# Optimization experiments

Hardware: AMD Instinct MI355X
Metric: run time of the kernel (lower is better)

The kernel has to match this reference:

```python
import jax, jax.numpy as jnp
import numpy as np

N = 100000
E = 1600000
DIN, DH, DOUT = 128, 128, 64


def setup_inputs() -> dict:
    key = jax.random.key(0)
    ks = jax.random.split(key, 9)
    x = jax.random.normal(ks[0], (N, DIN), dtype=jnp.float32)
    src = jax.random.randint(ks[1], (E,), 0, N, dtype=jnp.int32)
    dst = jax.random.randint(ks[2], (E,), 0, N, dtype=jnp.int32)
    edge_index = jnp.stack([src, dst])  # [2, E]

    def glorot(k, fi, fo):
        return jax.random.normal(k, (fi, fo), jnp.float32) * (1.0 / np.sqrt(fi))

    return {
        "x": x,
        "edge_index": edge_index,
        "W1": glorot(ks[3], DIN, DH), "b1": jnp.zeros((DH,), jnp.float32),
        "W2": glorot(ks[4], DH, DH),  "b2": jnp.zeros((DH,), jnp.float32),
        "W3": glorot(ks[5], DH, DOUT), "b3": jnp.zeros((DOUT,), jnp.float32),
    }


def _norm_and_edges(edge_index):
    # GCNConv: add self-loops, symmetric normalization D^{-1/2} (A+I) D^{-1/2}
    loop = jnp.arange(N, dtype=edge_index.dtype)
    src = jnp.concatenate([edge_index[0], loop])  # [E+N]
    dst = jnp.concatenate([edge_index[1], loop])
    deg = jax.ops.segment_sum(jnp.ones_like(dst, jnp.float32), dst, num_segments=N)
    dinv = jnp.where(deg > 0, jax.lax.rsqrt(jnp.maximum(deg, 1.0)), 0.0)
    norm = dinv[src] * dinv[dst]  # [E+N]
    return src, dst, norm


def _gcn_conv(x, W, b, src, dst, norm):
    h = x @ W                                   # [N, dout]
    msg = h[src] * norm[:, None]                # gather + scale over edges
    agg = jax.ops.segment_sum(msg, dst, num_segments=N)
    return agg + b


def reference(x, edge_index, W1, b1, W2, b2, W3, b3):
    src, dst, norm = _norm_and_edges(edge_index)
    out = []
    h = jax.nn.relu(_gcn_conv(x, W1, b1, src, dst, norm))
    out.append(h)
    h = jax.nn.relu(_gcn_conv(h, W2, b2, src, dst, norm))
    out.append(h)
    y = _gcn_conv(h, W3, b3, src, dst, norm)
    return (y, *out)
```

## Files before the change

kernel.cpp:

```cpp
#include <hip/hip_runtime.h>
#include <math.h>


typedef __attribute__((ext_vector_type(8))) short bfrag8;
typedef __attribute__((ext_vector_type(4))) float ffrag4;

__device__ __forceinline__ unsigned short f2bf(float f) {
  unsigned u = __float_as_uint(f);
  return (unsigned short)((u + 0x7FFFu + ((u >> 16) & 1u)) >> 16);
}
__device__ __forceinline__ float bfLo(unsigned v) { return __uint_as_float(v << 16); }
__device__ __forceinline__ float bfHi(unsigned v) { return __uint_as_float(v & 0xFFFF0000u); }


__global__ __launch_bounds__(256) void k_zero(int* __restrict__ cnt,
                                              int* __restrict__ fillPos, int n) {
  int i = blockIdx.x * blockDim.x + threadIdx.x;
  if (i < n) { cnt[i] = 0; fillPos[i] = 0; }
}

__global__ __launch_bounds__(256) void k_deg(const int* __restrict__ dst,
                                             int* __restrict__ cnt, int E) {
  int i = blockIdx.x * blockDim.x + threadIdx.x;
  int stride = gridDim.x * blockDim.x;
  for (; i < E; i += stride) atomicAdd(&cnt[dst[i]], 1);
}

__global__ __launch_bounds__(256) void k_dinv(const int* __restrict__ cnt,
                                              float* __restrict__ dinv, int n) {
  int i = blockIdx.x * blockDim.x + threadIdx.x;
  if (i < n) dinv[i] = rsqrtf(1.0f + (float)cnt[i]);
}

__global__ __launch_bounds__(256) void k_scan1(const int* __restrict__ cnt,
                                               int* __restrict__ exc,
                                               int* __restrict__ bsum, int n) {
  __shared__ int lds[256];
  int t = threadIdx.x;
  int base = blockIdx.x * 1024 + t * 4;
  int v0 = (base + 0 < n) ? cnt[base + 0] : 0;
  int v1 = (base + 1 < n) ? cnt[base + 1] : 0;
  int v2 = (base + 2 < n) ? cnt[base + 2] : 0;
  int v3 = (base + 3 < n) ? cnt[base + 3] : 0;
  int sum = v0 + v1 + v2 + v3;
  lds[t] = sum;
  __syncthreads();
  for (int off = 1; off < 256; off <<= 1) {
    int val = lds[t];
    if (t >= off) val += lds[t - off];
    __syncthreads();
    lds[t] = val;
    __syncthreads();
  }
  int ex = lds[t] - sum;
  if (base + 0 < n) exc[base + 0] = ex;
  ex += v0;
  if (base + 1 < n) exc[base + 1] = ex;
  ex += v1;
  if (base + 2 < n) exc[base + 2] = ex;
  ex += v2;
  if (base + 3 < n) exc[base + 3] = ex;
  if (t == 255) bsum[blockIdx.x] = lds[255];
}

__global__ __launch_bounds__(128) void k_scan2(int* __restrict__ bsum, int nb) {
  __shared__ int lds[128];
  int t = threadIdx.x;
  int v = (t < nb) ? bsum[t] : 0;
  lds[t] = v;
  __syncthreads();
  for (int off = 1; off < 128; off <<= 1) {
    int val = lds[t];
    if (t >= off) val += lds[t - off];
    __syncthreads();
    lds[t] = val;
    __syncthreads();
  }
  if (t < nb) bsum[t] = lds[t] - v;
}

__global__ __launch_bounds__(256) void k_scan3(int* __restrict__ exc,
                                               const int* __restrict__ bsum, int n) {
  int i = blockIdx.x * blockDim.x + threadIdx.x;
  if (i < n) exc[i] += bsum[i >> 10];
}

__global__ __launch_bounds__(256) void k_fill8(const int* __restrict__ src,
                                               const int* __restrict__ dst,
                                               const int* __restrict__ rowStart,
                                               int* __restrict__ fillPos,
                                               int* __restrict__ eSrc,
                                               int E, int rsize) {
  const int range = blockIdx.x & 7;
  const int sub = blockIdx.x >> 3;
  const int nSub = gridDim.x >> 3;
  const int lo = range * rsize, hi = lo + rsize;
  int i = sub * blockDim.x + threadIdx.x;
  const int stride = nSub * blockDim.x;
  for (; i < E; i += stride) {
    int d = dst[i];
    if (d >= lo && d < hi) {
      int p = rowStart[d] + atomicAdd(&fillPos[d], 1);
      eSrc[p] = src[i];
    }
  }
}


__global__ __launch_bounds__(256) void k_scale(const float* __restrict__ h,
                                               const float* __restrict__ dinv,
                                               uint4* __restrict__ s4, int nQuads) {
  int i = blockIdx.x * blockDim.x + threadIdx.x;
  int stride = gridDim.x * blockDim.x;
  for (; i < nQuads; i += stride) {
    int row = i >> 4;
    int q = i & 15;
    float dv = dinv[row];
    const float4* hp = (const float4*)&h[(size_t)row * 128 + 8 * q];
    float4 a = hp[0], b = hp[1];
    uint4 o;
    o.x = (unsigned)f2bf(dv * a.x) | ((unsigned)f2bf(dv * a.y) << 16);
    o.y = (unsigned)f2bf(dv * a.z) | ((unsigned)f2bf(dv * a.w) << 16);
    o.z = (unsigned)f2bf(dv * b.x) | ((unsigned)f2bf(dv * b.y) << 16);
    o.w = (unsigned)f2bf(dv * b.z) | ((unsigned)f2bf(dv * b.w) << 16);
    s4[i] = o;
  }
}

__global__ __launch_bounds__(256, 8) void k_agg(const unsigned* __restrict__ sU,
                                                const float* __restrict__ dinv,
                                                const int* __restrict__ eSrc,
                                                const int* __restrict__ rowStart,
                                                const int* __restrict__ cnt,
                                                unsigned* __restrict__ tB, int n) {
  const int wid = threadIdx.x >> 6, lane = threadIdx.x & 63;
  const int half = lane >> 5, sl = lane & 31;
  for (int node = blockIdx.x * 4 + wid; node < n; node += gridDim.x * 4) {
    const int st = rowStart[node], c = cnt[node];
    const int* es = eSrc + st;
    const float dv = dinv[node];
    uint2 vs = *(const uint2*)&sU[(size_t)node * 64 + 2 * sl];
    float a0, a1, a2, a3;
    if (half == 0) {
      a0 = bfLo(vs.x); a1 = bfHi(vs.x); a2 = bfLo(vs.y); a3 = bfHi(vs.y);
    } else {
      a0 = a1 = a2 = a3 = 0.f;
    }
    const int cl = c < 64 ? c : 64;
    int myIdx = (lane < cl) ? es[lane] : 0;
    int j = 0;
    for (; j + 8 <= cl; j += 8) {
      int iA0 = __shfl(myIdx, j + 0), iB0 = __shfl(myIdx, j + 1);
      int iA1 = __shfl(myIdx, j + 2), iB1 = __shfl(myIdx, j + 3);
      int iA2 = __shfl(myIdx, j + 4), iB2 = __shfl(myIdx, j + 5);
      int iA3 = __shfl(myIdx, j + 6), iB3 = __shfl(myIdx, j + 7);
      int x0 = half ? iB0 : iA0;
      int x1 = half ? iB1 : iA1;
      int x2 = half ? iB2 : iA2;
      int x3 = half ? iB3 : iA3;
      uint2 v0 = *(const uint2*)&sU[(size_t)x0 * 64 + 2 * sl];
      uint2 v1 = *(const uint2*)&sU[(size_t)x1 * 64 + 2 * sl];
      uint2 v2 = *(const uint2*)&sU[(size_t)x2 * 64 + 2 * sl];
      uint2 v3 = *(const uint2*)&sU[(size_t)x3 * 64 + 2 * sl];
      a0 += bfLo(v0.x); a1 += bfHi(v0.x); a2 += bfLo(v0.y); a3 += bfHi(v0.y);
      a0 += bfLo(v1.x); a1 += bfHi(v1.x); a2 += bfLo(v1.y); a3 += bfHi(v1.y);
      a0 += bfLo(v2.x); a1 += bfHi(v2.x); a2 += bfLo(v2.y); a3 += bfHi(v2.y);
      a0 += bfLo(v3.x); a1 += bfHi(v3.x); a2 += bfLo(v3.y); a3 += bfHi(v3.y);
    }
    for (; j < c; j += 2) {
      int iA = (j < cl) ? __shfl(myIdx, j) : es[j];
      int hasB = (j + 1 < c);
      int iB = hasB ? ((j + 1 < cl) ? __shfl(myIdx, j + 1) : es[j + 1]) : iA;
      int x = half ? iB : iA;
      uint2 v = *(const uint2*)&sU[(size_t)x * 64 + 2 * sl];
      if (half && !hasB) { v.x = 0u; v.y = 0u; }
      a0 += bfLo(v.x); a1 += bfHi(v.x); a2 += bfLo(v.y); a3 += bfHi(v.y);
    }
    a0 += __shfl_xor(a0, 32);
    a1 += __shfl_xor(a1, 32);
    a2 += __shfl_xor(a2, 32);
    a3 += __shfl_xor(a3, 32);
    if (half == 0) {
      uint2 o;
      o.x = (unsigned)f2bf(dv * a0) | ((unsigned)f2bf(dv * a1) << 16);
      o.y = (unsigned)f2bf(dv * a2) | ((unsigned)f2bf(dv * a3) << 16);
      *(uint2*)&tB[(size_t)node * 64 + 2 * sl] = o;
    }
  }
}

template <int NFO, bool RELU, bool WRITE_S>
__global__ __launch_bounds__(256) void k_gemmM(const unsigned* __restrict__ tB,
                                               const float* __restrict__ W,
                                               const float* __restrict__ bias,
                                               const float* __restrict__ dinv,
                                               float* __restrict__ out,
                                               unsigned* __restrict__ sNext, int n) {
  __shared__ unsigned short Wt[NFO * 128];
  for (int t = threadIdx.x; t < 128 * NFO; t += 256) {
    int k = t / NFO, c = t % NFO;
    int hs = (k >> 2) ^ (c & 7);
    Wt[c * 128 + hs * 4 + (k & 3)] = f2bf(W[t]);
  }
  __syncthreads();
  const int wid = threadIdx.x >> 6, lane = threadIdx.x & 63;
  const int r16 = lane & 15;
  const int q4 = lane >> 4;
  const int NT = NFO / 16;
  for (int node0 = (blockIdx.x * 4 + wid) * 16; node0 < n;
       node0 += gridDim.x * 4 * 16) {
    if (node0 + 16 <= n) {
      const unsigned* trow = tB + (size_t)(node0 + r16) * 64;
      union { uint2 u2[2]; bfrag8 v; } Af[4];
      #pragma unroll
      for (int kc = 0; kc < 4; kc++) {
        Af[kc].u2[0] = *(const uint2*)&trow[kc * 16 + 2 * q4];
        Af[kc].u2[1] = *(const uint2*)&trow[kc * 16 + 8 + 2 * q4];
      }
      float dvr[4];
      if (WRITE_S) {
        #pragma unroll
        for (int r = 0; r < 4; r++) dvr[r] = dinv[node0 + q4 * 4 + r];
      }
      #pragma unroll
      for (int ct = 0; ct < NT; ct++) {
        const int col = 16 * ct + r16;
        const int cbase = col * 128;
        const int csw = col & 7;
        ffrag4 acc = {0.f, 0.f, 0.f, 0.f};
        #pragma unroll
        for (int kc = 0; kc < 4; kc++) {
          int h0 = kc * 8 + q4;
          union { uint2 u2[2]; bfrag8 v; } Bf;
          Bf.u2[0] = *(const uint2*)&Wt[cbase + ((h0) ^ csw) * 4];
          Bf.u2[1] = *(const uint2*)&Wt[cbase + ((h0 + 4) ^ csw) * 4];
          acc = __builtin_amdgcn_mfma_f32_16x16x32_bf16(Af[kc].v, Bf.v, acc,
                                                        0, 0, 0);
        }
        float bb = bias[col];
        #pragma unroll
        for (int r = 0; r < 4; r++) {
          int node = node0 + q4 * 4 + r;
          float v = acc[r] + bb;
          if (RELU) v = fmaxf(v, 0.f);
          out[(size_t)node * NFO + col] = v;
          if (WRITE_S) {
            float sv = dvr[r] * v;
            float pv = __shfl_xor(sv, 1);
            if ((lane & 1) == 0)
              sNext[(size_t)node * 64 + (col >> 1)] =
                  (unsigned)f2bf(sv) | ((unsigned)f2bf(pv) << 16);
          }
        }
      }
    } else {
      for (int idx = lane; idx < 16 * NFO; idx += 64) {
        int node = node0 + idx / NFO;
        if (node < n) {
          int col = idx % NFO;
          float acc = 0.f;
          for (int k = 0; k < 128; k++) {
            unsigned tw = tB[(size_t)node * 64 + (k >> 1)];
            float tv = (k & 1) ? bfHi(tw) : bfLo(tw);
            int hs = (k >> 2) ^ (col & 7);
            unsigned short wv = Wt[col * 128 + hs * 4 + (k & 3)];
            acc = fmaf(tv, __uint_as_float(((unsigned)wv) << 16), acc);
          }
          float v = acc + bias[col];
          if (RELU) v = fmaxf(v, 0.f);
          out[(size_t)node * NFO + col] = v;
          if (WRITE_S) {
            unsigned short* sh = (unsigned short*)sNext;
            sh[(size_t)node * 128 + col] = f2bf(dinv[node] * v);
          }
        }
      }
    }
  }
}


template <int NFO, bool RELU>
__global__ __launch_bounds__(512) void k_layer_f32(const float* __restrict__ in,
                                                   const float* __restrict__ W,
                                                   const float* __restrict__ bias,
                                                   const float* __restrict__ dinv,
                                                   const int* __restrict__ eSrc,
                                                   const int* __restrict__ rowStart,
                                                   const int* __restrict__ cnt,
                                                   float* __restrict__ out, int n) {
  __shared__ float Wl[128 * NFO];
  for (int t = threadIdx.x; t < 128 * NFO; t += 512) Wl[t] = W[t];
  __syncthreads();
  const int wid = threadIdx.x >> 6, lane = threadIdx.x & 63;
  for (int node = blockIdx.x * 8 + wid; node < n; node += gridDim.x * 8) {
    const int s = rowStart[node], c = cnt[node];
    const int* es = eSrc + s;
    const float dv = dinv[node];
    float2 x2 = *(const float2*)&in[(size_t)node * 128 + 2 * lane];
    float ax = dv * x2.x, ay = dv * x2.y;
    int j = 0;
    for (; j + 4 <= c; j += 4) {
      int s0 = es[j], s1 = es[j + 1], s2 = es[j + 2], s3 = es[j + 3];
      float d0 = dinv[s0], d1 = dinv[s1], d2 = dinv[s2], d3 = dinv[s3];
      float2 v0 = *(const float2*)&in[(size_t)s0 * 128 + 2 * lane];
      float2 v1 = *(const float2*)&in[(size_t)s1 * 128 + 2 * lane];
      float2 v2 = *(const float2*)&in[(size_t)s2 * 128 + 2 * lane];
      float2 v3 = *(const float2*)&in[(size_t)s3 * 128 + 2 * lane];
      ax = fmaf(d0, v0.x, ax); ay = fmaf(d0, v0.y, ay);
      ax = fmaf(d1, v1.x, ax); ay = fmaf(d1, v1.y, ay);
      ax = fmaf(d2, v2.x, ax); ay = fmaf(d2, v2.y, ay);
      ax = fmaf(d3, v3.x, ax); ay = fmaf(d3, v3.y, ay);
    }
    for (; j < c; j++) {
      int sj = es[j];
      float dj = dinv[sj];
      float2 v = *(const float2*)&in[(size_t)sj * 128 + 2 * lane];
      ax = fmaf(dj, v.x, ax); ay = fmaf(dj, v.y, ay);
    }
    ax *= dv; ay *= dv;
    if constexpr (NFO == 128) {
      float o0 = 0.f, o1 = 0.f;
      #pragma unroll 4
      for (int kk = 0; kk < 64; kk++) {
        float xa = __shfl(ax, kk);
        float xb = __shfl(ay, kk);
        float2 wA = *(const float2*)&Wl[(2 * kk) * 128 + 2 * lane];
        float2 wB = *(const float2*)&Wl[(2 * kk + 1) * 128 + 2 * lane];
        o0 = fmaf(xa, wA.x, o0); o1 = fmaf(xa, wA.y, o1);
        o0 = fmaf(xb, wB.x, o0); o1 = fmaf(xb, wB.y, o1);
      }
      float2 bb = *(const float2*)&bias[2 * lane];
      float r0 = o0 + bb.x, r1 = o1 + bb.y;
      if (RELU) { r0 = fmaxf(r0, 0.f); r1 = fmaxf(r1, 0.f); }
      *(float2*)&out[(size_t)node * 128 + 2 * lane] = make_float2(r0, r1);
    } else {
      float o0 = 0.f;
      #pragma unroll 4
      for (int kk = 0; kk < 64; kk++) {
        float xa = __shfl(ax, kk);
        float xb = __shfl(ay, kk);
        o0 = fmaf(xa, Wl[(2 * kk) * NFO + lane], o0);
        o0 = fmaf(xb, Wl[(2 * kk + 1) * NFO + lane], o0);
      }
      float r0 = o0 + bias[lane];
      if (RELU) r0 = fmaxf(r0, 0.f);
      out[(size_t)node * NFO + lane] = r0;
    }
  }
}


extern "C" void kernel_launch(void* const* d_in, const int* in_sizes, int n_in,
                              void* d_out, int out_size, void* d_ws, size_t ws_size,
                              hipStream_t stream) {
  const float* x  = (const float*)d_in[0];
  const int*   ei = (const int*)d_in[1];
  const float* W1 = (const float*)d_in[2];
  const float* b1 = (const float*)d_in[3];
  const float* W2 = (const float*)d_in[4];
  const float* b2 = (const float*)d_in[5];
  const float* W3 = (const float*)d_in[6];
  const float* b3 = (const float*)d_in[7];

  const int N = in_sizes[0] / 128;
  const int E = in_sizes[1] / 2;
  const int* src = ei;
  const int* dst = ei + E;

  char* ws = (char*)d_ws;
  size_t off = 0;
  auto alloc = [&](size_t bytes) -> void* {
    void* p = ws + off;
    off = (off + bytes + 255) & ~(size_t)255;
    return p;
  };
  int*   cnt      = (int*)alloc((size_t)N * 4);
  int*   fillPos  = (int*)alloc((size_t)N * 4);
  int*   rowStart = (int*)alloc((size_t)N * 4);
  float* dinv     = (float*)alloc((size_t)N * 4);
  int*   bsum     = (int*)alloc(512);
  int*   eSrc     = (int*)alloc((size_t)E * 4);
  unsigned* sU    = (unsigned*)alloc((size_t)N * 64 * 4);
  unsigned* tB    = (unsigned*)alloc((size_t)N * 64 * 4);
  const bool fast = (ws_size >= off);

  float* y    = (float*)d_out;
  float* out1 = y + (size_t)N * 64;
  float* out2 = out1 + (size_t)N * 128;

  k_zero<<<(N + 255) / 256, 256, 0, stream>>>(cnt, fillPos, N);
  k_deg<<<2048, 256, 0, stream>>>(dst, cnt, E);
  k_dinv<<<(N + 255) / 256, 256, 0, stream>>>(cnt, dinv, N);
  int nChunks = (N + 1023) / 1024;
  k_scan1<<<nChunks, 256, 0, stream>>>(cnt, rowStart, bsum, N);
  k_scan2<<<1, 128, 0, stream>>>(bsum, nChunks);
  k_scan3<<<(N + 255) / 256, 256, 0, stream>>>(rowStart, bsum, N);
  const int rsize = (N + 7) / 8;
  k_fill8<<<2048, 256, 0, stream>>>(src, dst, rowStart, fillPos, eSrc, E, rsize);

  if (fast) {
    const int aggBlocks = (N + 3) / 4;
    const int tiles = (N + 15) / 16;
    const int gmBlocks = (tiles + 3) / 4;
    k_scale<<<(N * 16 + 255) / 256, 256, 0, stream>>>(x, dinv, (uint4*)sU, N * 16);
    k_agg<<<aggBlocks, 256, 0, stream>>>(sU, dinv, eSrc, rowStart, cnt, tB, N);
    k_gemmM<128, true, true><<<gmBlocks, 256, 0, stream>>>(tB, W1, b1, dinv, out1, sU, N);
    k_agg<<<aggBlocks, 256, 0, stream>>>(sU, dinv, eSrc, rowStart, cnt, tB, N);
    k_gemmM<128, true, true><<<gmBlocks, 256, 0, stream>>>(tB, W2, b2, dinv, out2, sU, N);
    k_agg<<<aggBlocks, 256, 0, stream>>>(sU, dinv, eSrc, rowStart, cnt, tB, N);
    k_gemmM<64, false, false><<<gmBlocks, 256, 0, stream>>>(tB, W3, b3, dinv, y, nullptr, N);
  } else {
    k_layer_f32<128, true ><<<1024, 512, 0, stream>>>(x,    W1, b1, dinv, eSrc, rowStart, cnt, out1, N);
    k_layer_f32<128, true ><<<1024, 512, 0, stream>>>(out1, W2, b2, dinv, eSrc, rowStart, cnt, out2, N);
    k_layer_f32<64,  false><<<1024, 512, 0, stream>>>(out2, W3, b3, dinv, eSrc, rowStart, cnt, y,    N);
  }
}
```

Before: 439.0 us.

## Pre-bucket edges by destination range and XCD before degree count and CSR fill

```diff
diff --git a/kernel.cpp b/kernel.cpp
--- a/kernel.cpp
+++ b/kernel.cpp
@@ -4,6 +4,8 @@
 
 typedef __attribute__((ext_vector_type(8))) short bfrag8;
 typedef __attribute__((ext_vector_type(4))) float ffrag4;
+
+static constexpr int BCAP = 32768;
 
 __device__ __forceinline__ unsigned short f2bf(float f) {
   unsigned u = __float_as_uint(f);
@@ -19,11 +21,111 @@
   if (i < n) { cnt[i] = 0; fillPos[i] = 0; }
 }
 
-__global__ __launch_bounds__(256) void k_deg(const int* __restrict__ dst,
-                                             int* __restrict__ cnt, int E) {
+__global__ __launch_bounds__(256) void k_zctr(int* __restrict__ c, int m) {
   int i = blockIdx.x * blockDim.x + threadIdx.x;
-  int stride = gridDim.x * blockDim.x;
-  for (; i < E; i += stride) atomicAdd(&cnt[dst[i]], 1);
+  if (i < m) c[i] = 0;
+}
+
+__global__ __launch_bounds__(256) void k_bucket(const int* __restrict__ src,
+                                                const int* __restrict__ dst,
+                                                uint2* __restrict__ buckets,
+                                                uint2* __restrict__ spill,
+                                                int* __restrict__ ctr,
+                                                int E, float invR) {
+  const int xcd = blockIdx.x & 7;
+  const int lane = threadIdx.x & 63;
+  int i = blockIdx.x * blockDim.x + threadIdx.x;
+  int iw = i - lane;
+  const int stride = gridDim.x * blockDim.x;
+  for (; iw < E; iw += stride, i += stride) {
+    bool valid = i < E;
+    int d = 0, s = 0, r = -1;
+    if (valid) {
+      d = dst[i];
+      s = src[i];
+      r = (int)((float)d * invR);
+      r = r > 7 ? 7 : r;
+    }
+    #pragma unroll
+    for (int rr = 0; rr < 8; rr++) {
+      unsigned long long m = __ballot(valid && (r == rr));
+      if (m) {
+        int cnum = __builtin_popcountll(m);
+        int leader = __builtin_ctzll(m);
+        int base = 0;
+        if (lane == leader) base = atomicAdd(&ctr[(rr * 8 + xcd) * 16], cnum);
+        base = __shfl(base, leader);
+        if (valid && r == rr) {
+          int off = __builtin_popcountll(m & ((1ull << lane) - 1ull));
+          int pos = base + off;
+          if (pos < BCAP) {
+            buckets[(size_t)(rr * 8 + xcd) * BCAP + pos] =
+                make_uint2((unsigned)s, (unsigned)d);
+          } else {
+            int sp = atomicAdd(&ctr[64 * 16], 1);
+            spill[sp] = make_uint2((unsigned)s, (unsigned)d);
+          }
+        }
+      }
+    }
+  }
+}
+
+__global__ __launch_bounds__(256) void k_deg8b(const uint2* __restrict__ buckets,
+                                               const uint2* __restrict__ spill,
+                                               const int* __restrict__ ctr,
+                                               int* __restrict__ cnt, float invR) {
+  const int range = blockIdx.x & 7;
+  const int sub = blockIdx.x >> 3;
+  const int nSub = gridDim.x >> 3;
+  const int tid = sub * blockDim.x + threadIdx.x;
+  const int stride = nSub * blockDim.x;
+  #pragma unroll
+  for (int x = 0; x < 8; x++) {
+    int m = ctr[(range * 8 + x) * 16];
+    m = m > BCAP ? BCAP : m;
+    const uint2* b = buckets + (size_t)(range * 8 + x) * BCAP;
+    for (int i = tid; i < m; i += stride) atomicAdd(&cnt[b[i].y], 1);
+  }
+  int sm = ctr[64 * 16];
+  for (int i = tid; i < sm; i += stride) {
+    unsigned d = spill[i].y;
+    int r = (int)((float)d * invR); r = r > 7 ? 7 : r;
+    if (r == range) atomicAdd(&cnt[d], 1);
+  }
+}
+
+__global__ __launch_bounds__(256) void k_fill8b(const uint2* __restrict__ buckets,
+                                                const uint2* __restrict__ spill,
+                                                const int* __restrict__ ctr,
+                                                const int* __restrict__ rowStart,
+                                                int* __restrict__ fillPos,
+                                                int* __restrict__ eSrc, float invR) {
+  const int range = blockIdx.x & 7;
+  const int sub = blockIdx.x >> 3;
+  const int nSub = gridDim.x >> 3;
+  const int tid = sub * blockDim.x + threadIdx.x;
+  const int stride = nSub * blockDim.x;
+  #pragma unroll
+  for (int x = 0; x < 8; x++) {
+    int m = ctr[(range * 8 + x) * 16];
+    m = m > BCAP ? BCAP : m;
+    const uint2* b = buckets + (size_t)(range * 8 + x) * BCAP;
+    for (int i = tid; i < m; i += stride) {
+      uint2 e = b[i];
+      int p = rowStart[e.y] + atomicAdd(&fillPos[e.y], 1);
+      eSrc[p] = (int)e.x;
+    }
+  }
+  int sm = ctr[64 * 16];
+  for (int i = tid; i < sm; i += stride) {
+    uint2 e = spill[i];
+    int r = (int)((float)e.y * invR); r = r > 7 ? 7 : r;
+    if (r == range) {
+      int p = rowStart[e.y] + atomicAdd(&fillPos[e.y], 1);
+      eSrc[p] = (int)e.x;
+    }
+  }
 }
 
 __global__ __launch_bounds__(256) void k_dinv(const int* __restrict__ cnt,
@@ -83,27 +185,6 @@
                                                const int* __restrict__ bsum, int n) {
   int i = blockIdx.x * blockDim.x + threadIdx.x;
   if (i < n) exc[i] += bsum[i >> 10];
-}
-
-__global__ __launch_bounds__(256) void k_fill8(const int* __restrict__ src,
-                                               const int* __restrict__ dst,
-                                               const int* __restrict__ rowStart,
-                                               int* __restrict__ fillPos,
-                                               int* __restrict__ eSrc,
-                                               int E, int rsize) {
-  const int range = blockIdx.x & 7;
-  const int sub = blockIdx.x >> 3;
-  const int nSub = gridDim.x >> 3;
-  const int lo = range * rsize, hi = lo + rsize;
-  int i = sub * blockDim.x + threadIdx.x;
-  const int stride = nSub * blockDim.x;
-  for (; i < E; i += stride) {
-    int d = dst[i];
-    if (d >= lo && d < hi) {
-      int p = rowStart[d] + atomicAdd(&fillPos[d], 1);
-      eSrc[p] = src[i];
-    }
-  }
 }
 
 
@@ -380,26 +461,34 @@
   int*   rowStart = (int*)alloc((size_t)N * 4);
   float* dinv     = (float*)alloc((size_t)N * 4);
   int*   bsum     = (int*)alloc(512);
+  int*   ctr      = (int*)alloc((64 * 16 + 16) * 4);
   int*   eSrc     = (int*)alloc((size_t)E * 4);
   unsigned* sU    = (unsigned*)alloc((size_t)N * 64 * 4);
   unsigned* tB    = (unsigned*)alloc((size_t)N * 64 * 4);
   const bool fast = (ws_size >= off);
 
+  uint2* buckets = (uint2*)tB;
+  uint2* spill   = (uint2*)sU;
+
   float* y    = (float*)d_out;
   float* out1 = y + (size_t)N * 64;
   float* out2 = out1 + (size_t)N * 128;
 
-  k_zero<<<(N + 255) / 256, 256, 0, stream>>>(cnt, fillPos, N);
-  k_deg<<<2048, 256, 0, stream>>>(dst, cnt, E);
-  k_dinv<<<(N + 255) / 256, 256, 0, stream>>>(cnt, dinv, N);
-  int nChunks = (N + 1023) / 1024;
-  k_scan1<<<nChunks, 256, 0, stream>>>(cnt, rowStart, bsum, N);
-  k_scan2<<<1, 128, 0, stream>>>(bsum, nChunks);
-  k_scan3<<<(N + 255) / 256, 256, 0, stream>>>(rowStart, bsum, N);
   const int rsize = (N + 7) / 8;
-  k_fill8<<<2048, 256, 0, stream>>>(src, dst, rowStart, fillPos, eSrc, E, rsize);
+  const float invR = (float)(1.0 / (double)rsize);
 
   if (fast) {
+    k_zero<<<(N + 255) / 256, 256, 0, stream>>>(cnt, fillPos, N);
+    k_zctr<<<5, 256, 0, stream>>>(ctr, 64 * 16 + 16);
+    k_bucket<<<2048, 256, 0, stream>>>(src, dst, buckets, spill, ctr, E, invR);
+    k_deg8b<<<2048, 256, 0, stream>>>(buckets, spill, ctr, cnt, invR);
+    k_dinv<<<(N + 255) / 256, 256, 0, stream>>>(cnt, dinv, N);
+    int nChunks = (N + 1023) / 1024;
+    k_scan1<<<nChunks, 256, 0, stream>>>(cnt, rowStart, bsum, N);
+    k_scan2<<<1, 128, 0, stream>>>(bsum, nChunks);
+    k_scan3<<<(N + 255) / 256, 256, 0, stream>>>(rowStart, bsum, N);
+    k_fill8b<<<2048, 256, 0, stream>>>(buckets, spill, ctr, rowStart, fillPos,
+                                       eSrc, invR);
     const int aggBlocks = (N + 3) / 4;
     const int tiles = (N + 15) / 16;
     const int gmBlocks = (tiles + 3) / 4;
@@ -411,6 +500,17 @@
     k_agg<<<aggBlocks, 256, 0, stream>>>(sU, dinv, eSrc, rowStart, cnt, tB, N);
     k_gemmM<64, false, false><<<gmBlocks, 256, 0, stream>>>(tB, W3, b3, dinv, y, nullptr, N);
   } else {
+    k_zero<<<(N + 255) / 256, 256, 0, stream>>>(cnt, fillPos, N);
+    k_zctr<<<5, 256, 0, stream>>>(ctr, 64 * 16 + 16);
+    k_bucket<<<2048, 256, 0, stream>>>(src, dst, buckets, spill, ctr, E, invR);
+    k_deg8b<<<2048, 256, 0, stream>>>(buckets, spill, ctr, cnt, invR);
+    k_dinv<<<(N + 255) / 256, 256, 0, stream>>>(cnt, dinv, N);
+    int nChunks = (N + 1023) / 1024;
+    k_scan1<<<nChunks, 256, 0, stream>>>(cnt, rowStart, bsum, N);
+    k_scan2<<<1, 128, 0, stream>>>(bsum, nChunks);
+    k_scan3<<<(N + 255) / 256, 256, 0, stream>>>(rowStart, bsum, N);
+    k_fill8b<<<2048, 256, 0, stream>>>(buckets, spill, ctr, rowStart, fillPos,
+                                       eSrc, invR);
     k_layer_f32<128, true ><<<1024, 512, 0, stream>>>(x,    W1, b1, dinv, eSrc, rowStart, cnt, out1, N);
     k_layer_f32<128, true ><<<1024, 512, 0, stream>>>(out1, W2, b2, dinv, eSrc, rowStart, cnt, out2, N);
     k_layer_f32<64,  false><<<1024, 512, 0, stream>>>(out2, W3, b3, dinv, eSrc, rowStart, cnt, y,    N);
```

New measurement: 541.8 us. 1.23x slower.
